# Performance work log

Hardware: AMD Instinct MI355X
Metric: run time of the kernel (lower is better)

Reference implementation:

```python
import jax, jax.numpy as jnp
import numpy as np

STRIDE = 16
NUM_A = 9
POS_TH, NEG_TH = 0.7, 0.3
FG, BG, IGN = 1.0, 0.0, 2.0
CAP = 128  # BATCH_SIZE * 0.5 for both fg and bg


def _generate_base_anchors(base_size=16, ratios=(0.5, 1.0, 2.0), scales=(8, 16, 32)):
    w = h = float(base_size)
    xc = yc = 0.5 * (base_size - 1)
    size = w * h
    out = []
    for r in ratios:
        ws = np.round(np.sqrt(size / r))
        hs = np.round(ws * r)
        for s in scales:
            W, H = ws * s, hs * s
            out.append([xc - 0.5 * (W - 1), yc - 0.5 * (H - 1),
                        xc + 0.5 * (W - 1), yc + 0.5 * (H - 1)])
    return np.asarray(out, dtype=np.float32)  # [9,4]


def _all_anchors(H, W):
    base = _generate_base_anchors()
    sx = np.arange(W, dtype=np.float32) * STRIDE
    sy = np.arange(H, dtype=np.float32) * STRIDE
    xs, ys = np.meshgrid(sx, sy)  # row-major over (h, w)
    shifts = np.stack([xs.ravel(), ys.ravel(), xs.ravel(), ys.ravel()], 1)
    return jnp.asarray((shifts[:, None, :] + base[None, :, :]).reshape(-1, 4))  # [H*W*9,4], order (h,w,a)


def _forward(scores, gt, im_w, im_h):
    H, W = scores.shape[2], scores.shape[3]
    anchors = _all_anchors(H, W)  # [N,4]
    valid = (anchors[:, 0] >= 0.) & (anchors[:, 1] >= 0.) & \
            (anchors[:, 2] < im_w) & (anchors[:, 3] < im_h)
    # pairwise IoU with +1 box convention
    aw = anchors[:, 2] - anchors[:, 0] + 1.
    ah = anchors[:, 3] - anchors[:, 1] + 1.
    a_area = jnp.where((aw > 0) & (ah > 0), aw * ah, 0.)
    gw = gt[:, 2] - gt[:, 0] + 1.
    gh = gt[:, 3] - gt[:, 1] + 1.
    g_area = jnp.where((gw > 0) & (gh > 0), gw * gh, 0.)
    ix1 = jnp.maximum(anchors[:, None, 0], gt[None, :, 0])
    iy1 = jnp.maximum(anchors[:, None, 1], gt[None, :, 1])
    ix2 = jnp.minimum(anchors[:, None, 2], gt[None, :, 2])
    iy2 = jnp.minimum(anchors[:, None, 3], gt[None, :, 3])
    iw = ix2 - ix1 + 1.
    ih = iy2 - iy1 + 1.
    inter = jnp.where((iw > 0) & (ih > 0), iw * ih, 0.)
    ovl = inter / (a_area[:, None] + g_area[None, :] - inter)  # [N,G]
    ovl_m = jnp.where(valid[:, None], ovl, -1.)  # exclude invalid anchors
    a_argmax = jnp.argmax(ovl, axis=1)           # best gt per anchor
    a_max = jnp.max(ovl, axis=1)
    g_max = jnp.max(ovl_m, axis=0)               # best (valid) anchor overlap per gt
    gt_fg = jnp.any(ovl_m == g_max[None, :], axis=1) & valid
    labels = jnp.where(valid & (a_max < NEG_TH), BG, IGN)
    labels = jnp.where(gt_fg, FG, labels)
    labels = jnp.where(valid & (a_max >= POS_TH), FG, labels)
    # random subsample fg/bg down to CAP each (matches npr.choice semantics in distribution)
    kf, kb = jax.random.split(jax.random.key(42))
    def subsample(lbl, mask, k):
        s = jnp.where(mask, jax.random.uniform(k, lbl.shape), jnp.inf)
        ranks = jnp.argsort(jnp.argsort(s))
        keep = ranks < jnp.minimum(jnp.sum(mask), CAP)
        return jnp.where(mask & ~keep, IGN, lbl)
    labels = subsample(labels, labels == FG, kf)
    labels = subsample(labels, labels == BG, kb)
    num_ni = jnp.sum(labels != IGN).astype(jnp.float32)
    gts = gt[a_argmax]
    ax = (anchors[:, 2] + anchors[:, 0]) * 0.5
    ay = (anchors[:, 3] + anchors[:, 1]) * 0.5
    gwm = gts[:, 2] - gts[:, 0] + 1.
    ghm = gts[:, 3] - gts[:, 1] + 1.
    gx = (gts[:, 2] + gts[:, 0]) * 0.5
    gy = (gts[:, 3] + gts[:, 1]) * 0.5
    adj = jnp.stack([(gx - ax) / aw, (gy - ay) / ah,
                     jnp.log(gwm / aw), jnp.log(ghm / ah)], axis=1)  # [N,4]
    adj = jnp.where(valid[:, None], adj, 0.)
    wts = jnp.where((labels == FG)[:, None], 1.0 / num_ni, 0.) * jnp.ones((1, 4), jnp.float32)
    labels_out = labels.reshape(1, H, W, NUM_A).transpose(0, 3, 1, 2) \
                       .reshape(1, 1, NUM_A * H, W).astype(jnp.int32)
    adj_out = adj.reshape(1, H, W, 4 * NUM_A).transpose(0, 3, 1, 2)
    wts_out = wts.reshape(1, H, W, 4 * NUM_A).transpose(0, 3, 1, 2)
    return labels_out, adj_out, wts_out


def setup_inputs() -> dict:
    key = jax.random.key(0)
    k1, k2, k3 = jax.random.split(key, 3)
    scores = jax.random.normal(k1, (1, 18, 256, 256), dtype=jnp.float32)
    G = 64
    cxy = jax.random.uniform(k2, (G, 2), minval=100., maxval=3900.)
    wh = jax.random.uniform(k3, (G, 2), minval=32., maxval=512.)
    x1y1 = jnp.clip(cxy - wh * 0.5, 0., 4095.)
    x2y2 = jnp.clip(cxy + wh * 0.5, 0., 4095.)
    gt = jnp.concatenate([x1y1, x2y2], axis=1)  # [G,4] = x1,y1,x2,y2
    return {"anchor_object_scores": scores, "ground_truth_boxes": gt,
            "im_w": 4096, "im_h": 4096}


def reference(anchor_object_scores, ground_truth_boxes, im_w, im_h):
    return _forward(anchor_object_scores, ground_truth_boxes, im_w, im_h)
```

## Files before the change

### kernel.cpp

```cpp
#include <hip/hip_runtime.h>
#include <stdint.h>


#define NUM_A 9
#define HW 65536
#define N_ANCH 589824
#define NG 64
#define CAPK 128u
#define NBIN 2048
#define BIN_SHIFT 12
#define CAND_CAP 4096

#define LAB_BG 0u
#define LAB_FG 1u
#define LAB_IGN 2u

#define OFF_GMAX8 0
#define OFF_HF    512
#define OFF_HB    (OFF_HF + NBIN)
#define OFF_CNTF  (OFF_HF + 2*NBIN)
#define OFF_CNTB  (OFF_CNTF + 1)
#define OFF_DONE2 (OFF_CNTF + 2)
#define OFF_SEL   (OFF_CNTF + 4)
#define OFF_CANDF 4620
#define OFF_CANDB (OFF_CANDF + 2*CAND_CAP)
#define OFF_LABM  (OFF_CANDB + 2*CAND_CAP)
#define ZERO_BEG  OFF_HF
#define ZERO_END  OFF_CANDF
#define NZ        (ZERO_END - ZERO_BEG)

__constant__ float BA[NUM_A][4] = {
  { -84.f,  -40.f,  99.f,  55.f}, {-176.f,  -88.f, 191.f, 103.f},
  {-360.f, -184.f, 375.f, 199.f}, { -56.f,  -56.f,  71.f,  71.f},
  {-120.f, -120.f, 135.f, 135.f}, {-248.f, -248.f, 263.f, 263.f},
  { -36.f,  -80.f,  51.f,  95.f}, { -80.f, -168.f,  95.f, 183.f},
  {-168.f, -344.f, 183.f, 359.f}};

__host__ __device__ static inline void tf2x32(uint32_t k0, uint32_t k1,
                                              uint32_t x0, uint32_t x1,
                                              uint32_t* o0, uint32_t* o1) {
  const uint32_t ks2 = k0 ^ k1 ^ 0x1BD11BDAu;
#define TF_R(r) { x0 += x1; x1 = (x1 << (r)) | (x1 >> (32 - (r))); x1 ^= x0; }
  x0 += k0; x1 += k1;
  TF_R(13) TF_R(15) TF_R(26) TF_R(6)
  x0 += k1;  x1 += ks2 + 1u;
  TF_R(17) TF_R(29) TF_R(16) TF_R(24)
  x0 += ks2; x1 += k0 + 2u;
  TF_R(13) TF_R(15) TF_R(26) TF_R(6)
  x0 += k0;  x1 += k1 + 3u;
  TF_R(17) TF_R(29) TF_R(16) TF_R(24)
  x0 += k1;  x1 += ks2 + 4u;
  TF_R(13) TF_R(15) TF_R(26) TF_R(6)
  x0 += ks2; x1 += k0 + 5u;
#undef TF_R
  *o0 = x0; *o1 = x1;
}

__device__ static inline uint32_t mant_of(uint32_t k0, uint32_t k1, uint32_t n) {
  uint32_t o0, o1;
  tf2x32(k0, k1, 0u, n, &o0, &o1);
  return (o0 ^ o1) >> 9;
}

__device__ static inline float iou1(float a0, float a1, float a2, float a3,
                                    float aarea, float g0, float g1, float g2,
                                    float g3, float garea) {
  #pragma clang fp contract(off)
  float ix1 = fmaxf(a0, g0);
  float iy1 = fmaxf(a1, g1);
  float ix2 = fminf(a2, g2);
  float iy2 = fminf(a3, g3);
  float iw = ix2 - ix1 + 1.0f;
  float ih = iy2 - iy1 + 1.0f;
  float inter = (iw > 0.0f && ih > 0.0f) ? iw * ih : 0.0f;
  float den = aarea + garea - inter;
  return inter / den;
}

__global__ __launch_bounds__(256) void k_gmax(const float* __restrict__ gt,
                                              const int* __restrict__ imw_p,
                                              const int* __restrict__ imh_p,
                                              uint32_t* __restrict__ ws) {
  #pragma clang fp contract(off)
  int tid = threadIdx.x;
  int b = blockIdx.x;
  int gid = b * 256 + tid;
  if (gid < NZ) ws[ZERO_BEG + gid] = 0u;

  int g = b >> 3, sl = b & 7;
  float g0 = gt[g*4+0], g1 = gt[g*4+1], g2 = gt[g*4+2], g3 = gt[g*4+3];
  float gw = g2 - g0 + 1.0f, gh = g3 - g1 + 1.0f;
  float ga = (gw > 0.0f && gh > 0.0f) ? gw * gh : 0.0f;
  float imw = (float)imw_p[0], imh = (float)imh_p[0];

  float mx = 0.0f;
  for (int a = 0; a < NUM_A; a++) {
    float b0 = BA[a][0], b1 = BA[a][1], b2 = BA[a][2], b3 = BA[a][3];
    int wlo = max(0,   (int)floorf((g0 - 1.0f - b2) * 0.0625f));
    int whi = min(255, (int)ceilf ((g2 + 1.0f - b0) * 0.0625f));
    int hlo = max(0,   (int)floorf((g1 - 1.0f - b3) * 0.0625f));
    int hhi = min(255, (int)ceilf ((g3 + 1.0f - b1) * 0.0625f));
    int wx = whi - wlo + 1, wy = hhi - hlo + 1;
    if (wx <= 0 || wy <= 0) continue;
    int tot = wx * wy;
    for (int idx = sl * 256 + tid; idx < tot; idx += 2048) {
      int h = hlo + idx / wx, w = wlo + idx % wx;
      float sx = (float)(w << 4), sy = (float)(h << 4);
      float x1 = b0 + sx, y1 = b1 + sy, x2 = b2 + sx, y2 = b3 + sy;
      float aw = x2 - x1 + 1.0f, ah = y2 - y1 + 1.0f;
      float aarea = aw * ah;
      bool vld = (x1 >= 0.0f) && (y1 >= 0.0f) && (x2 < imw) && (y2 < imh);
      float o = iou1(x1, y1, x2, y2, aarea, g0, g1, g2, g3, ga);
      if (vld) mx = fmaxf(mx, o);
    }
  }
  #pragma unroll
  for (int s = 32; s >= 1; s >>= 1) mx = fmaxf(mx, __shfl_xor(mx, s, 64));
  __shared__ float wmax[4];
  if ((tid & 63) == 0) wmax[tid >> 6] = mx;
  __syncthreads();
  if (tid == 0) {
    float m = fmaxf(fmaxf(wmax[0], wmax[1]), fmaxf(wmax[2], wmax[3]));
    ws[OFF_GMAX8 + g * 8 + sl] = __float_as_uint(m);
  }
}

__global__ __launch_bounds__(256) void k_main(const float* __restrict__ gt,
                                              const int* __restrict__ imw_p,
                                              const int* __restrict__ imh_p,
                                              float* __restrict__ out_adj,
                                              uint32_t* __restrict__ ws,
                                              uint32_t kf0, uint32_t kf1,
                                              uint32_t kb0, uint32_t kb1) {
  #pragma clang fp contract(off)
  __shared__ float sg0[NG], sg1[NG], sg2[NG], sg3[NG], sga[NG], sgm[NG];
  __shared__ uint32_t sh[2 * NBIN];
  __shared__ unsigned long long sMask[4];
  __shared__ int sAnyZero, sLast;
  int tid = threadIdx.x;
  {
    uint4* sh4 = (uint4*)sh;
    #pragma unroll
    for (int k = 0; k < 4; k++) sh4[tid + k * 256] = make_uint4(0, 0, 0, 0);
  }
  if (tid == 0) sAnyZero = 0;
  if (tid < NG) {
    const float4 g4 = ((const float4*)gt)[tid];
    sg0[tid] = g4.x; sg1[tid] = g4.y; sg2[tid] = g4.z; sg3[tid] = g4.w;
    float gw = g4.z - g4.x + 1.0f, gh = g4.w - g4.y + 1.0f;
    sga[tid] = (gw > 0.0f && gh > 0.0f) ? gw * gh : 0.0f;
    uint32_t mm = 0u;
    #pragma unroll
    for (int j = 0; j < 8; j++) mm = max(mm, ws[OFF_GMAX8 + tid * 8 + j]);
    sgm[tid] = __uint_as_float(mm);
    if (mm == 0u) atomicOr(&sAnyZero, 1);
  }
  __syncthreads();

  int b = blockIdx.x;
  int a = b >> 6, hb = (b & 63) << 2;
  float BA0 = BA[a][0], BA1 = BA[a][1], BA2 = BA[a][2], BA3 = BA[a][3];

  {
    int wv = tid >> 6, g = tid & 63;
    float sy = (float)((hb + wv) << 4);
    float ihp = fminf(BA3 + sy, sg3[g]) - fmaxf(BA1 + sy, sg1[g]) + 1.0f;
    unsigned long long mk = __ballot(ihp > 0.0f);
    if (g == 0) sMask[wv] = mk;
  }
  __syncthreads();

  float imw = (float)imw_p[0], imh = (float)imh_p[0];
  int w = tid;
  float sx = (float)(w << 4);
  float A0 = BA0 + sx, A2 = BA2 + sx;
  float aw = A2 - A0 + 1.0f;
  float A1v[4], A3v[4];
  #pragma unroll
  for (int r = 0; r < 4; r++) {
    float sy = (float)((hb + r) << 4);
    A1v[r] = BA1 + sy; A3v[r] = BA3 + sy;
  }
  float ah = A3v[0] - A1v[0] + 1.0f;
  float aarea = aw * ah;
  bool xv = (A0 >= 0.0f) && (A2 < imw);

  unsigned long long mk0 = sMask[0], mk1 = sMask[1],
                     mk2 = sMask[2], mk3 = sMask[3];
  unsigned long long uni = mk0 | mk1 | mk2 | mk3;
  float amaxv[4] = {0.f, 0.f, 0.f, 0.f};
  int bgv[4] = {0, 0, 0, 0};
  uint32_t afv = 0u;
  while (uni) {
    int g = __ffsll(uni) - 1;
    uni &= uni - 1;
    float iw = fminf(A2, sg2[g]) - fmaxf(A0, sg0[g]) + 1.0f;
    if (!__any(iw > 0.0f)) continue;
    if (iw > 0.0f) {
      float base = aarea + sga[g];
      float gy1 = sg1[g], gy2 = sg3[g], gm = sgm[g];
#define DO_ROW(r, mk)                                                     \
      if ((mk >> g) & 1ull) {                                             \
        float ih = fminf(A3v[r], gy2) - fmaxf(A1v[r], gy1) + 1.0f;        \
        float inter = iw * ih;                                            \
        float o = inter / (base - inter);                                 \
        if (o > amaxv[r]) { amaxv[r] = o; bgv[r] = g; }                   \
        if (o == gm) afv |= (1u << r);                                    \
      }
      DO_ROW(0, mk0) DO_ROW(1, mk1) DO_ROW(2, mk2) DO_ROW(3, mk3)
#undef DO_ROW
    }
  }

  bool anyZ = (sAnyZero != 0);
  #pragma unroll
  for (int r = 0; r < 4; r++) {
    int hw = (hb + r) * 256 + w;
    bool valid = xv && (A1v[r] >= 0.0f) && (A3v[r] < imh);
    float amax = amaxv[r];
    bool anyfg = (((afv >> r) & 1u) || anyZ) && valid;
    uint32_t lab;
    if (!valid)                       lab = LAB_IGN;
    else if (anyfg || amax >= 0.7f)   lab = LAB_FG;
    else if (amax < 0.3f)             lab = LAB_BG;
    else                              lab = LAB_IGN;

    float adj0 = 0.f, adj1 = 0.f, adj2 = 0.f, adj3 = 0.f;
    if (valid) {
      int bg = bgv[r];
      float G0 = sg0[bg], G1 = sg1[bg], G2 = sg2[bg], G3 = sg3[bg];
      float ax = (A2 + A0) * 0.5f, ay = (A3v[r] + A1v[r]) * 0.5f;
      float gwm = G2 - G0 + 1.0f, ghm = G3 - G1 + 1.0f;
      float gx = (G2 + G0) * 0.5f, gy = (G3 + G1) * 0.5f;
      adj0 = (gx - ax) / aw;
      adj1 = (gy - ay) / ah;
      adj2 = logf(gwm / aw);
      adj3 = logf(ghm / ah);
    }
    int c4 = a * 4;
    out_adj[(c4 + 0) * HW + hw] = adj0;
    out_adj[(c4 + 1) * HW + hw] = adj1;
    out_adj[(c4 + 2) * HW + hw] = adj2;
    out_adj[(c4 + 3) * HW + hw] = adj3;

    uint32_t m = 0u;
    uint32_t n = (uint32_t)(hw * 9 + a);
    if (lab != LAB_IGN) {
      uint32_t kk0 = (lab == LAB_FG) ? kf0 : kb0;
      uint32_t kk1 = (lab == LAB_FG) ? kf1 : kb1;
      m = mant_of(kk0, kk1, n);
      atomicAdd(&sh[((lab == LAB_FG) ? 0 : NBIN) + (m >> BIN_SHIFT)], 1u);
    }
    ws[OFF_LABM + a * HW + hw] = (lab << 24) | m;
  }

  __syncthreads();
  for (int i = tid; i < 2 * NBIN; i += 256) {
    uint32_t v = sh[i];
    if (v) atomicAdd(&ws[OFF_HF + i], v);
  }
  __syncthreads();
  if (tid == 0)
    sLast = (atomicAdd(&ws[OFF_DONE2], 1u) == 575u) ? 1 : 0;
  __syncthreads();
  if (sLast) {
    for (int cls = 0; cls < 2; cls++) {
      uint32_t* hist = ws + (cls ? OFF_HB : OFF_HF);
      uint32_t* sel = ws + OFF_SEL + cls * 4;
      uint32_t loc[8], s = 0;
      #pragma unroll
      for (int j = 0; j < 8; j++) {
        loc[j] = __hip_atomic_load(&hist[tid * 8 + j], __ATOMIC_RELAXED,
                                   __HIP_MEMORY_SCOPE_AGENT);
        s += loc[j];
      }
      sh[tid] = s; __syncthreads();
      for (int off = 1; off < 256; off <<= 1) {
        uint32_t v = (tid >= off) ? sh[tid - off] : 0u;
        __syncthreads();
        sh[tid] += v;
        __syncthreads();
      }
      uint32_t total = sh[255];
      uint32_t K = total < CAPK ? total : CAPK;
      if (tid == 0) {
        sel[3] = K;
        if (K == 0u) { sel[0] = 0xFFFFFFFFu; sel[1] = 0u; sel[2] = 0u; }
      }
      if (K > 0u) {
        uint32_t myC = sh[tid], pvC = (tid == 0) ? 0u : sh[tid - 1];
        if (myC >= K && pvC < K) {
          uint32_t cum = pvC; int bb = tid * 8;
          for (int j = 0; j < 8; j++) {
            if (cum + loc[j] >= K) { bb = tid * 8 + j; break; }
            cum += loc[j];
          }
          sel[0] = (uint32_t)bb; sel[1] = cum; sel[2] = K - cum;
        }
      }
      __syncthreads();
    }
  }
}

__global__ __launch_bounds__(256) void k_emit(float* __restrict__ out_lab,
                                              float* __restrict__ out_wts,
                                              uint32_t* __restrict__ ws) {
  int t = blockIdx.x * 256 + threadIdx.x;
  uint32_t lm = ws[OFF_LABM + t];
  uint32_t lab = lm >> 24;
  uint32_t m = lm & 0x7FFFFFu;
  uint32_t Kf = ws[OFF_SEL + 3], Kb = ws[OFF_SEL + 7];
  float inv = 1.0f / (float)(Kf + Kb);
  int a = t >> 16, hw = t & 65535;
  uint32_t n = (uint32_t)(hw * 9 + a);

  float outv = 2.0f, wv = 0.0f;
  if (lab == LAB_FG) {
    uint32_t b = m >> BIN_SHIFT, bf = ws[OFF_SEL + 0];
    if (b < bf) { outv = 1.0f; wv = inv; }
    else if (b == bf) {
      uint32_t idx = atomicAdd(&ws[OFF_CNTF], 1u);
      if (idx < CAND_CAP)
        ((uint64_t*)(ws + OFF_CANDF))[idx] = ((uint64_t)m << 20) | (uint64_t)n;
    }
  } else if (lab == LAB_BG) {
    uint32_t b = m >> BIN_SHIFT, bb = ws[OFF_SEL + 4];
    if (b < bb) { outv = 0.0f; }
    else if (b == bb) {
      uint32_t idx = atomicAdd(&ws[OFF_CNTB], 1u);
      if (idx < CAND_CAP)
        ((uint64_t*)(ws + OFF_CANDB))[idx] = ((uint64_t)m << 20) | (uint64_t)n;
    }
  }
  out_lab[t] = outv;
  int c4 = a * 4;
  out_wts[(c4 + 0) * HW + hw] = wv;
  out_wts[(c4 + 1) * HW + hw] = wv;
  out_wts[(c4 + 2) * HW + hw] = wv;
  out_wts[(c4 + 3) * HW + hw] = wv;
}

__global__ __launch_bounds__(256) void k_fixup(float* __restrict__ out_lab,
                                               float* __restrict__ out_wts,
                                               uint32_t* __restrict__ ws) {
  __shared__ uint64_t sc[CAND_CAP];
  int cls = blockIdx.x;
  uint32_t cnt = ws[cls == 0 ? OFF_CNTF : OFF_CNTB];
  uint32_t C = cnt < CAND_CAP ? cnt : CAND_CAP;
  uint32_t need = ws[OFF_SEL + cls * 4 + 2];
  uint32_t Kf = ws[OFF_SEL + 3], Kb = ws[OFF_SEL + 7];
  float inv = 1.0f / (float)(Kf + Kb);
  const uint64_t* cand =
      (const uint64_t*)(ws + (cls == 0 ? OFF_CANDF : OFF_CANDB));
  for (uint32_t i = threadIdx.x; i < C; i += 256) sc[i] = cand[i];
  __syncthreads();
  for (uint32_t i = threadIdx.x; i < C; i += 256) {
    uint64_t k = sc[i];
    uint32_t r = 0;
    for (uint32_t j = 0; j < C; j++) r += (sc[j] < k) ? 1u : 0u;
    if (r < need) {
      uint32_t n = (uint32_t)(k & 0xFFFFFu);
      uint32_t a = n % 9u, hw = n / 9u;
      uint32_t t = a * HW + hw;
      if (cls == 0) {
        out_lab[t] = 1.0f;
        #pragma unroll
        for (int j = 0; j < 4; j++) out_wts[(a * 4 + j) * HW + hw] = inv;
      } else {
        out_lab[t] = 0.0f;
      }
    }
  }
}

extern "C" void kernel_launch(void* const* d_in, const int* in_sizes, int n_in,
                              void* d_out, int out_size, void* d_ws,
                              size_t ws_size, hipStream_t stream) {
  const float* gt  = (const float*)d_in[1];
  const int*   imw = (const int*)d_in[2];
  const int*   imh = (const int*)d_in[3];
  float* out      = (float*)d_out;
  float* out_lab  = out;
  float* out_adj  = out + N_ANCH;
  float* out_wts  = out + 5 * N_ANCH;
  uint32_t* ws = (uint32_t*)d_ws;

  uint32_t kf0, kf1, kb0, kb1;
  tf2x32(0u, 42u, 0u, 0u, &kf0, &kf1);
  tf2x32(0u, 42u, 0u, 1u, &kb0, &kb1);

  hipLaunchKernelGGL(k_gmax, dim3(NG * 8), dim3(256), 0, stream, gt, imw, imh,
                     ws);
  hipLaunchKernelGGL(k_main, dim3(576), dim3(256), 0, stream, gt, imw, imh,
                     out_adj, ws, kf0, kf1, kb0, kb1);
  hipLaunchKernelGGL(k_emit, dim3(N_ANCH / 256), dim3(256), 0, stream, out_lab,
                     out_wts, ws);
  hipLaunchKernelGGL(k_fixup, dim3(2), dim3(256), 0, stream, out_lab, out_wts,
                     ws);
}
```

Before: 102.6 us.

## Fuse main, emit and fixup kernels into one persistent kernel with grid barriers

Merges the label/histogram kernel, the emit kernel and the fixup kernel into a single kernel. Each block keeps its per-anchor label and mantissa in registers instead of writing them to a workspace buffer and reading them back. Cross-block ordering is handled by atomic arrival counters, a release/acquire flag spin-wait, and a second barrier before two blocks run the candidate fixup. This removes two launches and the workspace round trip. It depends on all 576 blocks being co-resident (launch bounds set to 3 blocks per CU), otherwise the spin-waits could deadlock. The candidate capacity is also halved to fit the shared buffer.

Measured after the change: 194.3 us. 1.89x slower.

```diff
diff --git a/kernel.cpp b/kernel.cpp
--- a/kernel.cpp
+++ b/kernel.cpp
@@ -9,7 +9,8 @@
 #define CAPK 128u
 #define NBIN 2048
 #define BIN_SHIFT 12
-#define CAND_CAP 4096
+#define CAND_CAP 2048
+#define NBLK 576
 
 #define LAB_BG 0u
 #define LAB_FG 1u
@@ -20,11 +21,12 @@
 #define OFF_HB    (OFF_HF + NBIN)
 #define OFF_CNTF  (OFF_HF + 2*NBIN)
 #define OFF_CNTB  (OFF_CNTF + 1)
-#define OFF_DONE2 (OFF_CNTF + 2)
-#define OFF_SEL   (OFF_CNTF + 4)
-#define OFF_CANDF 4620
+#define OFF_ARR1  (OFF_CNTF + 2)
+#define OFF_ARR2  (OFF_CNTF + 3)
+#define OFF_FLAG  (OFF_CNTF + 4)
+#define OFF_SEL   (OFF_CNTF + 8)
+#define OFF_CANDF 4624
 #define OFF_CANDB (OFF_CANDF + 2*CAND_CAP)
-#define OFF_LABM  (OFF_CANDB + 2*CAND_CAP)
 #define ZERO_BEG  OFF_HF
 #define ZERO_END  OFF_CANDF
 #define NZ        (ZERO_END - ZERO_BEG)
@@ -77,10 +79,10 @@
   return inter / den;
 }
 
-__global__ __launch_bounds__(256) void k_gmax(const float* __restrict__ gt,
-                                              const int* __restrict__ imw_p,
-                                              const int* __restrict__ imh_p,
-                                              uint32_t* __restrict__ ws) {
+__global__ __launch_bounds__(256) void k_pre(const float* __restrict__ gt,
+                                             const int* __restrict__ imw_p,
+                                             const int* __restrict__ imh_p,
+                                             uint32_t* __restrict__ ws) {
   #pragma clang fp contract(off)
   int tid = threadIdx.x;
   int b = blockIdx.x;
@@ -125,18 +127,22 @@
   }
 }
 
-__global__ __launch_bounds__(256) void k_main(const float* __restrict__ gt,
-                                              const int* __restrict__ imw_p,
-                                              const int* __restrict__ imh_p,
-                                              float* __restrict__ out_adj,
-                                              uint32_t* __restrict__ ws,
-                                              uint32_t kf0, uint32_t kf1,
-                                              uint32_t kb0, uint32_t kb1) {
+__global__ __launch_bounds__(256, 3) void k_fat(const float* __restrict__ gt,
+                                                const int* __restrict__ imw_p,
+                                                const int* __restrict__ imh_p,
+                                                float* __restrict__ out_lab,
+                                                float* __restrict__ out_adj,
+                                                float* __restrict__ out_wts,
+                                                uint32_t* __restrict__ ws,
+                                                uint32_t kf0, uint32_t kf1,
+                                                uint32_t kb0, uint32_t kb1) {
   #pragma clang fp contract(off)
   __shared__ float sg0[NG], sg1[NG], sg2[NG], sg3[NG], sga[NG], sgm[NG];
-  __shared__ uint32_t sh[2 * NBIN];
+  __shared__ uint64_t sbuf[NBIN];
   __shared__ unsigned long long sMask[4];
   __shared__ int sAnyZero, sLast;
+  __shared__ uint32_t ssel[8];
+  uint32_t* sh = (uint32_t*)sbuf;
   int tid = threadIdx.x;
   {
     uint4* sh4 = (uint4*)sh;
@@ -213,6 +219,7 @@
   }
 
   bool anyZ = (sAnyZero != 0);
+  uint32_t labm[4];
   #pragma unroll
   for (int r = 0; r < 4; r++) {
     int hw = (hb + r) * 256 + w;
@@ -251,7 +258,7 @@
       m = mant_of(kk0, kk1, n);
       atomicAdd(&sh[((lab == LAB_FG) ? 0 : NBIN) + (m >> BIN_SHIFT)], 1u);
     }
-    ws[OFF_LABM + a * HW + hw] = (lab << 24) | m;
+    labm[r] = (lab << 24) | m;
   }
 
   __syncthreads();
@@ -260,13 +267,17 @@
     if (v) atomicAdd(&ws[OFF_HF + i], v);
   }
   __syncthreads();
-  if (tid == 0)
-    sLast = (atomicAdd(&ws[OFF_DONE2], 1u) == 575u) ? 1 : 0;
-  __syncthreads();
+  if (tid == 0) {
+    uint32_t prev = __hip_atomic_fetch_add(&ws[OFF_ARR1], 1u,
+                                           __ATOMIC_ACQ_REL,
+                                           __HIP_MEMORY_SCOPE_AGENT);
+    sLast = (prev == NBLK - 1u) ? 1 : 0;
+  }
+  __syncthreads();
+
   if (sLast) {
     for (int cls = 0; cls < 2; cls++) {
       uint32_t* hist = ws + (cls ? OFF_HB : OFF_HF);
-      uint32_t* sel = ws + OFF_SEL + cls * 4;
       uint32_t loc[8], s = 0;
       #pragma unroll
       for (int j = 0; j < 8; j++) {
@@ -283,9 +294,14 @@
       }
       uint32_t total = sh[255];
       uint32_t K = total < CAPK ? total : CAPK;
+      uint32_t* sel = ws + OFF_SEL + cls * 4;
       if (tid == 0) {
-        sel[3] = K;
-        if (K == 0u) { sel[0] = 0xFFFFFFFFu; sel[1] = 0u; sel[2] = 0u; }
+        __hip_atomic_store(&sel[3], K, __ATOMIC_RELAXED,
+                           __HIP_MEMORY_SCOPE_AGENT);
+        if (K == 0u) {
+          __hip_atomic_store(&sel[0], 0xFFFFFFFFu, __ATOMIC_RELAXED,
+                             __HIP_MEMORY_SCOPE_AGENT);
+        }
       }
       if (K > 0u) {
         uint32_t myC = sh[tid], pvC = (tid == 0) ? 0u : sh[tid - 1];
@@ -295,80 +311,108 @@
             if (cum + loc[j] >= K) { bb = tid * 8 + j; break; }
             cum += loc[j];
           }
-          sel[0] = (uint32_t)bb; sel[1] = cum; sel[2] = K - cum;
+          __hip_atomic_store(&sel[0], (uint32_t)bb, __ATOMIC_RELAXED,
+                             __HIP_MEMORY_SCOPE_AGENT);
+          __hip_atomic_store(&sel[1], cum, __ATOMIC_RELAXED,
+                             __HIP_MEMORY_SCOPE_AGENT);
+          __hip_atomic_store(&sel[2], K - cum, __ATOMIC_RELAXED,
+                             __HIP_MEMORY_SCOPE_AGENT);
         }
       }
       __syncthreads();
     }
-  }
-}
-
-__global__ __launch_bounds__(256) void k_emit(float* __restrict__ out_lab,
-                                              float* __restrict__ out_wts,
-                                              uint32_t* __restrict__ ws) {
-  int t = blockIdx.x * 256 + threadIdx.x;
-  uint32_t lm = ws[OFF_LABM + t];
-  uint32_t lab = lm >> 24;
-  uint32_t m = lm & 0x7FFFFFu;
-  uint32_t Kf = ws[OFF_SEL + 3], Kb = ws[OFF_SEL + 7];
+    if (tid == 0)
+      __hip_atomic_store(&ws[OFF_FLAG], 1u, __ATOMIC_RELEASE,
+                         __HIP_MEMORY_SCOPE_AGENT);
+  }
+
+  if (tid == 0) {
+    while (__hip_atomic_load(&ws[OFF_FLAG], __ATOMIC_ACQUIRE,
+                             __HIP_MEMORY_SCOPE_AGENT) == 0u)
+      __builtin_amdgcn_s_sleep(2);
+  }
+  __syncthreads();
+  if (tid < 8)
+    ssel[tid] = __hip_atomic_load(&ws[OFF_SEL + tid], __ATOMIC_RELAXED,
+                                  __HIP_MEMORY_SCOPE_AGENT);
+  __syncthreads();
+
+  uint32_t bf = ssel[0], bbs = ssel[4];
+  uint32_t Kf = ssel[3], Kb = ssel[7];
   float inv = 1.0f / (float)(Kf + Kb);
-  int a = t >> 16, hw = t & 65535;
-  uint32_t n = (uint32_t)(hw * 9 + a);
-
-  float outv = 2.0f, wv = 0.0f;
-  if (lab == LAB_FG) {
-    uint32_t b = m >> BIN_SHIFT, bf = ws[OFF_SEL + 0];
-    if (b < bf) { outv = 1.0f; wv = inv; }
-    else if (b == bf) {
-      uint32_t idx = atomicAdd(&ws[OFF_CNTF], 1u);
-      if (idx < CAND_CAP)
-        ((uint64_t*)(ws + OFF_CANDF))[idx] = ((uint64_t)m << 20) | (uint64_t)n;
-    }
-  } else if (lab == LAB_BG) {
-    uint32_t b = m >> BIN_SHIFT, bb = ws[OFF_SEL + 4];
-    if (b < bb) { outv = 0.0f; }
-    else if (b == bb) {
-      uint32_t idx = atomicAdd(&ws[OFF_CNTB], 1u);
-      if (idx < CAND_CAP)
-        ((uint64_t*)(ws + OFF_CANDB))[idx] = ((uint64_t)m << 20) | (uint64_t)n;
-    }
-  }
-  out_lab[t] = outv;
-  int c4 = a * 4;
-  out_wts[(c4 + 0) * HW + hw] = wv;
-  out_wts[(c4 + 1) * HW + hw] = wv;
-  out_wts[(c4 + 2) * HW + hw] = wv;
-  out_wts[(c4 + 3) * HW + hw] = wv;
-}
-
-__global__ __launch_bounds__(256) void k_fixup(float* __restrict__ out_lab,
-                                               float* __restrict__ out_wts,
-                                               uint32_t* __restrict__ ws) {
-  __shared__ uint64_t sc[CAND_CAP];
-  int cls = blockIdx.x;
-  uint32_t cnt = ws[cls == 0 ? OFF_CNTF : OFF_CNTB];
-  uint32_t C = cnt < CAND_CAP ? cnt : CAND_CAP;
-  uint32_t need = ws[OFF_SEL + cls * 4 + 2];
-  uint32_t Kf = ws[OFF_SEL + 3], Kb = ws[OFF_SEL + 7];
-  float inv = 1.0f / (float)(Kf + Kb);
-  const uint64_t* cand =
-      (const uint64_t*)(ws + (cls == 0 ? OFF_CANDF : OFF_CANDB));
-  for (uint32_t i = threadIdx.x; i < C; i += 256) sc[i] = cand[i];
-  __syncthreads();
-  for (uint32_t i = threadIdx.x; i < C; i += 256) {
-    uint64_t k = sc[i];
-    uint32_t r = 0;
-    for (uint32_t j = 0; j < C; j++) r += (sc[j] < k) ? 1u : 0u;
-    if (r < need) {
-      uint32_t n = (uint32_t)(k & 0xFFFFFu);
-      uint32_t a = n % 9u, hw = n / 9u;
-      uint32_t t = a * HW + hw;
-      if (cls == 0) {
-        out_lab[t] = 1.0f;
-        #pragma unroll
-        for (int j = 0; j < 4; j++) out_wts[(a * 4 + j) * HW + hw] = inv;
-      } else {
-        out_lab[t] = 0.0f;
+  uint64_t* candf = (uint64_t*)(ws + OFF_CANDF);
+  uint64_t* candb = (uint64_t*)(ws + OFF_CANDB);
+  #pragma unroll
+  for (int r = 0; r < 4; r++) {
+    int hw = (hb + r) * 256 + w;
+    uint32_t lab = labm[r] >> 24;
+    uint32_t m = labm[r] & 0x7FFFFFu;
+    uint32_t n = (uint32_t)(hw * 9 + a);
+    float outv = 2.0f, wv = 0.0f;
+    if (lab == LAB_FG) {
+      uint32_t bn = m >> BIN_SHIFT;
+      if (bn < bf) { outv = 1.0f; wv = inv; }
+      else if (bn == bf) {
+        uint32_t idx = atomicAdd(&ws[OFF_CNTF], 1u);
+        if (idx < CAND_CAP)
+          __hip_atomic_store(&candf[idx], ((uint64_t)m << 20) | (uint64_t)n,
+                             __ATOMIC_RELAXED, __HIP_MEMORY_SCOPE_AGENT);
+      }
+    } else if (lab == LAB_BG) {
+      uint32_t bn = m >> BIN_SHIFT;
+      if (bn < bbs) { outv = 0.0f; }
+      else if (bn == bbs) {
+        uint32_t idx = atomicAdd(&ws[OFF_CNTB], 1u);
+        if (idx < CAND_CAP)
+          __hip_atomic_store(&candb[idx], ((uint64_t)m << 20) | (uint64_t)n,
+                             __ATOMIC_RELAXED, __HIP_MEMORY_SCOPE_AGENT);
+      }
+    }
+    out_lab[a * HW + hw] = outv;
+    int c4 = a * 4;
+    out_wts[(c4 + 0) * HW + hw] = wv;
+    out_wts[(c4 + 1) * HW + hw] = wv;
+    out_wts[(c4 + 2) * HW + hw] = wv;
+    out_wts[(c4 + 3) * HW + hw] = wv;
+  }
+
+  __syncthreads();
+  if (tid == 0)
+    __hip_atomic_fetch_add(&ws[OFF_ARR2], 1u, __ATOMIC_ACQ_REL,
+                           __HIP_MEMORY_SCOPE_AGENT);
+  if (b < 2) {
+    if (tid == 0) {
+      while (__hip_atomic_load(&ws[OFF_ARR2], __ATOMIC_ACQUIRE,
+                               __HIP_MEMORY_SCOPE_AGENT) < (uint32_t)NBLK)
+        __builtin_amdgcn_s_sleep(2);
+    }
+    __syncthreads();
+    int cls = b;
+    uint32_t cnt = __hip_atomic_load(&ws[cls == 0 ? OFF_CNTF : OFF_CNTB],
+                                     __ATOMIC_RELAXED,
+                                     __HIP_MEMORY_SCOPE_AGENT);
+    uint32_t C = cnt < CAND_CAP ? cnt : CAND_CAP;
+    uint32_t need = ssel[cls * 4 + 2];
+    const uint64_t* cand = (cls == 0) ? candf : candb;
+    for (uint32_t i = tid; i < C; i += 256)
+      sbuf[i] = __hip_atomic_load(&cand[i], __ATOMIC_RELAXED,
+                                  __HIP_MEMORY_SCOPE_AGENT);
+    __syncthreads();
+    for (uint32_t i = tid; i < C; i += 256) {
+      uint64_t k = sbuf[i];
+      uint32_t r = 0;
+      for (uint32_t j = 0; j < C; j++) r += (sbuf[j] < k) ? 1u : 0u;
+      if (r < need) {
+        uint32_t n = (uint32_t)(k & 0xFFFFFu);
+        uint32_t aa = n % 9u, hw = n / 9u;
+        uint32_t t = aa * HW + hw;
+        if (cls == 0) {
+          out_lab[t] = 1.0f;
+          #pragma unroll
+          for (int j = 0; j < 4; j++) out_wts[(aa * 4 + j) * HW + hw] = inv;
+        } else {
+          out_lab[t] = 0.0f;
+        }
       }
     }
   }
@@ -390,12 +434,8 @@
   tf2x32(0u, 42u, 0u, 0u, &kf0, &kf1);
   tf2x32(0u, 42u, 0u, 1u, &kb0, &kb1);
 
-  hipLaunchKernelGGL(k_gmax, dim3(NG * 8), dim3(256), 0, stream, gt, imw, imh,
+  hipLaunchKernelGGL(k_pre, dim3(NG * 8), dim3(256), 0, stream, gt, imw, imh,
                      ws);
-  hipLaunchKernelGGL(k_main, dim3(576), dim3(256), 0, stream, gt, imw, imh,
-                     out_adj, ws, kf0, kf1, kb0, kb1);
-  hipLaunchKernelGGL(k_emit, dim3(N_ANCH / 256), dim3(256), 0, stream, out_lab,
-                     out_wts, ws);
-  hipLaunchKernelGGL(k_fixup, dim3(2), dim3(256), 0, stream, out_lab, out_wts,
-                     ws);
-}
+  hipLaunchKernelGGL(k_fat, dim3(NBLK), dim3(256), 0, stream, gt, imw, imh,
+                     out_lab, out_adj, out_wts, ws, kf0, kf1, kb0, kb1);
+}
```
